# Optimization experiments

Measured on AMD Instinct MI355X. Metric: run time of the kernel, lower is better.

The kernel has to match this reference:

```python
import jax, jax.numpy as jnp
import numpy as np

SIZES = [(64, 32), (32, 16), (16, 8), (8, 16), (16, 32)]
BZ, T, D = 2048, 512, 64


def setup_inputs() -> dict:
    key = jax.random.key(0)
    ks = jax.random.split(key, 32)
    inp = {
        "X": jax.random.normal(ks[0], (BZ, T, D), jnp.float32),
        "missing_mask": (jax.random.uniform(ks[1], (BZ, T, D)) < 0.8).astype(jnp.float32),
        "imputation_latent": jax.random.normal(ks[2], (BZ, T, D), jnp.float32),
    }
    for i, (din, dh) in enumerate(SIZES):
        s = 1.0 / np.sqrt(dh)  # PyTorch RNNCell init range
        k = 3 + 4 * i
        inp[f"wih{i}"] = jax.random.uniform(ks[k], (3 * dh, din), jnp.float32, -s, s)
        inp[f"whh{i}"] = jax.random.uniform(ks[k + 1], (3 * dh, dh), jnp.float32, -s, s)
        inp[f"bih{i}"] = jax.random.uniform(ks[k + 2], (3 * dh,), jnp.float32, -s, s)
        inp[f"bhh{i}"] = jax.random.uniform(ks[k + 3], (3 * dh,), jnp.float32, -s, s)
    so = 1.0 / np.sqrt(32)
    inp["out_w"] = jax.random.uniform(ks[23], (D, 32), jnp.float32, -so, so)
    inp["out_b"] = jax.random.uniform(ks[24], (D,), jnp.float32, -so, so)
    return inp


def _gru_cell(x, h, wih, whh, bih, bhh):
    # PyTorch nn.GRUCell gate order: r, z, n
    gi = x @ wih.T + bih
    gh = h @ whh.T + bhh
    ir, iz, inn = jnp.split(gi, 3, axis=-1)
    hr, hz, hn = jnp.split(gh, 3, axis=-1)
    r = jax.nn.sigmoid(ir + hr)
    z = jax.nn.sigmoid(iz + hz)
    n = jnp.tanh(inn + r * hn)
    return (1.0 - z) * n + z * h


def _forward(X, missing_mask, imputation_latent, params, out_w, out_b):
    imputed = X * missing_mask + imputation_latent * (1.0 - missing_mask)
    xs = jnp.swapaxes(imputed, 0, 1)  # [T, B, D]
    bz = X.shape[0]
    h0 = tuple(jnp.zeros((bz, dh), X.dtype) for _, dh in SIZES)

    def step(hs, x):
        new = []
        inp_x = x
        for i, (wih, whh, bih, bhh) in enumerate(params):
            h = _gru_cell(inp_x, hs[i], wih, whh, bih, bhh)
            new.append(h)
            inp_x = h  # layer i+1 consumes the freshly-updated hidden state
        return tuple(new), new[-1]

    _, hcol = jax.lax.scan(step, h0, xs)  # [T, B, 32]
    hcol = jnp.swapaxes(hcol, 0, 1)  # [B, T, 32]
    return hcol @ out_w.T + out_b


def reference(X, missing_mask, imputation_latent,
              wih0, whh0, bih0, bhh0, wih1, whh1, bih1, bhh1,
              wih2, whh2, bih2, bhh2, wih3, whh3, bih3, bhh3,
              wih4, whh4, bih4, bhh4, out_w, out_b):
    params = [(wih0, whh0, bih0, bhh0), (wih1, whh1, bih1, bhh1),
              (wih2, whh2, bih2, bhh2), (wih3, whh3, bih3, bhh3),
              (wih4, whh4, bih4, bhh4)]
    return _forward(X, missing_mask, imputation_latent, params, out_w, out_b)
```

## Files before the change

kernel.cpp:

```cpp
#include <hip/hip_runtime.h>

typedef short s16x8 __attribute__((ext_vector_type(8)));
typedef short s16x4 __attribute__((ext_vector_type(4)));
typedef float f32x4 __attribute__((ext_vector_type(4)));
typedef unsigned int u32;
typedef unsigned short u16;

#define NT 512
#define DD 64
#define BB 8
#define NTH 512

#define CHUNK 1024

#define P2STRIDE (5*CHUNK)
#define PH0 0
#define PH1 CHUNK
#define PH2 (2*CHUNK)
#define PH3 (3*CHUNK)
#define PH4 (4*CHUNK)
#define FRTOT2 (2*P2STRIDE)
#define NSTEP2 517

#define PSTRIDE (7*CHUNK)
#define XIN0 0
#define H0C (2*CHUNK)
#define H1C (3*CHUNK)
#define H2C (4*CHUNK)
#define H3C (5*CHUNK)
#define H4C (6*CHUNK)
#define FRTOT (2*PSTRIDE)
#define NSTEP_FB 517

#define MFMA16(A,B,C) __builtin_amdgcn_mfma_f32_16x16x32_bf16(A,B,C,0,0,0)

__device__ __forceinline__ float sigf(float x){ return 1.0f/(1.0f+__expf(-x)); }
__device__ __forceinline__ float tanhf2(float x){ return 2.0f/(1.0f+__expf(-2.0f*x)) - 1.0f; }

__device__ __forceinline__ u16 f2bf(float f) {
  u32 u = __builtin_bit_cast(u32, f);
  return (u16)((u + 0x7fffu + ((u >> 16) & 1u)) >> 16);
}
__device__ __forceinline__ float bf2f(u16 h) {
  u32 u = ((u32)h) << 16;
  return __builtin_bit_cast(float, u);
}

__device__ __forceinline__ void soft_barrier() {
  asm volatile("s_waitcnt lgkmcnt(0)" ::: "memory");
  __builtin_amdgcn_s_barrier();
  asm volatile("" ::: "memory");
}

__device__ __forceinline__ u32 cvtpk_bf16(float a, float b) {
  u32 r;
  asm("v_cvt_pk_bf16_f32 %0, %1, %2" : "=v"(r) : "v"(a), "v"(b));
  return r;
}

__device__ __forceinline__ void load_wfrag(const float* __restrict__ W, int row0, int nrow, int din,
                                           int kbase, int lane, s16x8& hi, s16x8& lo)
{
  const int m = lane & 15, kb = lane >> 4;
#pragma unroll
  for (int e = 0; e < 8; ++e) {
    int k = kbase + kb*8 + e;
    float v = (m < nrow && k < din) ? W[(size_t)(row0 + m)*din + k] : 0.0f;
    u16 h = f2bf(v);
    hi[e] = (short)h;
    lo[e] = (short)f2bf(v - bf2f(h));
  }
}

__device__ __forceinline__ void read_b(const u16* base, int lane, s16x8& hi, s16x8& lo)
{
  const int off = ((lane >> 4) << 8) + ((lane & 15) << 3);
  hi = *(const s16x8*)(base + off);
  lo = *(const s16x8*)(base + off + 128);
}

__device__ __forceinline__ void combine_write2(
    f32x4 aR, f32x4 aZ, f32x4 aNi, f32x4 aNh,
    float (&hprev)[4], u16* hdst_base, int jbase, int nrow, int lane)
{
  const int bb = lane & 15, q = lane >> 4;
  float hv[4];
#pragma unroll
  for (int i = 0; i < 4; ++i) {
    float rr = sigf(aR[i]);
    float zz = sigf(aZ[i]);
    float nn = tanhf2(aNi[i] + rr*aNh[i]);
    hv[i] = (1.0f - zz)*nn + zz*hprev[i];
    hprev[i] = hv[i];
  }
  if (bb < 8 && q*4 < nrow) {
    const int j = jbase + q*4;
    u16* dst = hdst_base + ((j >> 3) << 8) + bb*8 + (j & 7);
    u32 p01 = cvtpk_bf16(hv[0], hv[1]);
    u32 p23 = cvtpk_bf16(hv[2], hv[3]);
    float h0 = __builtin_bit_cast(float, p01 << 16);
    float h1 = __builtin_bit_cast(float, p01 & 0xffff0000u);
    float h2 = __builtin_bit_cast(float, p23 << 16);
    float h3 = __builtin_bit_cast(float, p23 & 0xffff0000u);
    u32 q01 = cvtpk_bf16(hv[0]-h0, hv[1]-h1);
    u32 q23 = cvtpk_bf16(hv[2]-h2, hv[3]-h3);
    uint2 hp_; hp_.x = p01; hp_.y = p23;
    uint2 lp_; lp_.x = q01; lp_.y = q23;
    *(uint2*)dst = hp_;
    *(uint2*)(dst + 128) = lp_;
  }
}

__device__ __forceinline__ void combine_write(
    f32x4 aR, f32x4 aZ, f32x4 aNi, f32x4 aNh,
    float (&hprev)[4], u16* hdst_base, int jbase, int nrow, int lane)
{
  const int bb = lane & 15, q = lane >> 4;
  float hv[4];
#pragma unroll
  for (int i = 0; i < 4; ++i) {
    float rr = sigf(aR[i]);
    float zz = sigf(aZ[i]);
    float nn = tanhf2(aNi[i] + rr*aNh[i]);
    hv[i] = (1.0f - zz)*nn + zz*hprev[i];
    hprev[i] = hv[i];
  }
  if (bb < 8 && q*4 < nrow) {
    const int j = jbase + q*4;
    const int kb = j >> 3, e = j & 7;
    s16x4 hh, ll;
#pragma unroll
    for (int i = 0; i < 4; ++i) {
      u16 h = f2bf(hv[i]);
      hh[i] = (short)h;
      ll[i] = (short)f2bf(hv[i] - bf2f(h));
    }
    u16* dst = hdst_base + kb*256 + bb*8 + e;
    *(s16x4*)dst = hh;
    *(s16x4*)(dst + 128) = ll;
  }
}

__global__ __launch_bounds__(256)
void gi0_gemm(const float* __restrict__ X, const float* __restrict__ M, const float* __restrict__ L,
              const float* __restrict__ wih0, const float* __restrict__ bih0,
              const float* __restrict__ bhh0,
              float* __restrict__ gi)
{
  __shared__ u32 xs[128*65];
  const int tid = threadIdx.x;
  const int wv = tid >> 6, lane = tid & 63;
  const int q = lane >> 4;
  const int b = blockIdx.x >> 2;
  const int t0 = (blockIdx.x & 3) * 128;
  const size_t base = ((size_t)b*NT + t0)*DD;

  for (int i = tid; i < 128*64; i += 256) {
    float x = X[base+i], m = M[base+i], l = L[base+i];
    float v = x*m + l*(1.0f - m);
    u16 h = f2bf(v);
    u16 lo2 = f2bf(v - bf2f(h));
    const int t = i >> 6, d = i & 63;
    xs[t*65 + d] = (u32)h | ((u32)lo2 << 16);
  }

  s16x8 Ah[6][2], Al[6][2];
  f32x4 cb[6];
#pragma unroll
  for (int tile = 0; tile < 6; ++tile) {
#pragma unroll
    for (int c = 0; c < 2; ++c)
      load_wfrag(wih0, tile*16, 16, 64, c*32, lane, Ah[tile][c], Al[tile][c]);
#pragma unroll
    for (int i = 0; i < 4; ++i) {
      int row = tile*16 + q*4 + i;
      float bv = bih0[row];
      if (tile < 4) bv += bhh0[row];
      cb[tile][i] = bv;
    }
  }
  __syncthreads();

#pragma unroll
  for (int g2 = 0; g2 < 2; ++g2) {
    const int tloc = g2*64 + wv*16 + (lane & 15);
    s16x8 Bh[2], Bl[2];
#pragma unroll
    for (int c = 0; c < 2; ++c) {
      const u32* p = &xs[tloc*65 + c*32 + q*8];
#pragma unroll
      for (int e = 0; e < 8; ++e) {
        u32 v = p[e];
        Bh[c][e] = (short)(v & 0xffffu);
        Bl[c][e] = (short)(v >> 16);
      }
    }
    float* gp = gi + ((size_t)b*NT + t0 + tloc)*96 + q*4;
#pragma unroll
    for (int tile = 0; tile < 6; ++tile) {
      f32x4 acc = cb[tile];
#pragma unroll
      for (int c = 0; c < 2; ++c) {
        acc = MFMA16(Ah[tile][c], Bh[c], acc);
        acc = MFMA16(Ah[tile][c], Bl[c], acc);
        acc = MFMA16(Al[tile][c], Bh[c], acc);
      }
      *(f32x4*)(gp + tile*16) = acc;
    }
  }
}

__device__ __forceinline__ void wave_l0(
    const float* __restrict__ Whh, const float* __restrict__ bhh,
    const float* __restrict__ gi, int jbase,
    u16* FRu, int b0, int lane)
{
  s16x8 Ahh[3], Ahl[3];
#pragma unroll
  for (int g = 0; g < 3; ++g)
    load_wfrag(Whh, g*32 + jbase, 16, 32, 0, lane, Ahh[g], Ahl[g]);
  const int q = lane >> 4;
  f32x4 cNh;
#pragma unroll
  for (int i = 0; i < 4; ++i) cNh[i] = bhh[64 + jbase + q*4 + i];
  float hprev[4] = {0.f,0.f,0.f,0.f};

  const float* gp = gi + (size_t)(b0 + (lane & 7)) * ((size_t)NT*96) + jbase + q*4;
  f32x4 gR0, gZ0, gN0, gR1, gZ1, gN1;
  gR0 = *(const f32x4*)(gp); gZ0 = *(const f32x4*)(gp+32); gN0 = *(const f32x4*)(gp+64); gp += 96;
  gR1 = *(const f32x4*)(gp); gZ1 = *(const f32x4*)(gp+32); gN1 = *(const f32x4*)(gp+64); gp += 96;

  for (int s = 0; s < NSTEP2; ++s) {
    const int par = s & 1, rp = par ^ 1;
    f32x4 gR2 = {}, gZ2 = {}, gN2 = {};
    if (s + 2 < NT) {
      gR2 = *(const f32x4*)(gp); gZ2 = *(const f32x4*)(gp+32); gN2 = *(const f32x4*)(gp+64); gp += 96;
    }
    if (s < NT) {
      f32x4 aR = gR0, aZ = gZ0, aNi = gN0, aNh = cNh;
      s16x8 bh_, bl_;
      read_b(FRu + rp*P2STRIDE + PH0, lane, bh_, bl_);
      aR  = MFMA16(Ahh[0], bh_, aR);  aR  = MFMA16(Ahh[0], bl_, aR);  aR  = MFMA16(Ahl[0], bh_, aR);
      aZ  = MFMA16(Ahh[1], bh_, aZ);  aZ  = MFMA16(Ahh[1], bl_, aZ);  aZ  = MFMA16(Ahl[1], bh_, aZ);
      aNh = MFMA16(Ahh[2], bh_, aNh); aNh = MFMA16(Ahh[2], bl_, aNh); aNh = MFMA16(Ahl[2], bh_, aNh);
      combine_write2(aR, aZ, aNi, aNh, hprev, FRu + par*P2STRIDE + PH0, jbase, 16, lane);
    }
    gR0 = gR1; gZ0 = gZ1; gN0 = gN1;
    gR1 = gR2; gZ1 = gZ2; gN1 = gN2;
    soft_barrier();
  }
}

template<int DIN, int DH>
__device__ __forceinline__ void wave_mid(
    const float* __restrict__ Wih, const float* __restrict__ Whh,
    const float* __restrict__ bih, const float* __restrict__ bhh,
    int jbase, int xc, int hc, int s0, int s1,
    u16* FRu, int b0, int lane)
{
  const int nrow = (DH - jbase) < 16 ? (DH - jbase) : 16;
  s16x8 Axh[3], Axl[3], Ahh[3], Ahl[3];
#pragma unroll
  for (int g = 0; g < 3; ++g) {
    load_wfrag(Wih, g*DH + jbase, nrow, DIN, 0, lane, Axh[g], Axl[g]);
    load_wfrag(Whh, g*DH + jbase, nrow, DH, 0, lane, Ahh[g], Ahl[g]);
  }
  const int q = lane >> 4;
  f32x4 cR, cZ, cNi, cNh;
#pragma unroll
  for (int i = 0; i < 4; ++i) {
    int lr = q*4 + i;
    int j = jbase + lr;
    bool jr = lr < nrow;
    cR[i]  = jr ? bih[j] + bhh[j] : 0.f;
    cZ[i]  = jr ? bih[DH+j] + bhh[DH+j] : 0.f;
    cNi[i] = jr ? bih[2*DH+j] : 0.f;
    cNh[i] = jr ? bhh[2*DH+j] : 0.f;
  }
  float hprev[4] = {0.f,0.f,0.f,0.f};

  for (int s = 0; s < NSTEP2; ++s) {
    const int par = s & 1, rp = par ^ 1;
    if (s >= s0 && s <= s1) {
      f32x4 aR = cR, aZ = cZ, aNi = cNi, aNh = cNh;
      s16x8 bh_, bl_;
      read_b(FRu + rp*P2STRIDE + xc, lane, bh_, bl_);
      aR  = MFMA16(Axh[0], bh_, aR);  aR  = MFMA16(Axh[0], bl_, aR);  aR  = MFMA16(Axl[0], bh_, aR);
      aZ  = MFMA16(Axh[1], bh_, aZ);  aZ  = MFMA16(Axh[1], bl_, aZ);  aZ  = MFMA16(Axl[1], bh_, aZ);
      aNi = MFMA16(Axh[2], bh_, aNi); aNi = MFMA16(Axh[2], bl_, aNi); aNi = MFMA16(Axl[2], bh_, aNi);
      read_b(FRu + rp*P2STRIDE + hc, lane, bh_, bl_);
      aR  = MFMA16(Ahh[0], bh_, aR);  aR  = MFMA16(Ahh[0], bl_, aR);  aR  = MFMA16(Ahl[0], bh_, aR);
      aZ  = MFMA16(Ahh[1], bh_, aZ);  aZ  = MFMA16(Ahh[1], bl_, aZ);  aZ  = MFMA16(Ahl[1], bh_, aZ);
      aNh = MFMA16(Ahh[2], bh_, aNh); aNh = MFMA16(Ahh[2], bl_, aNh); aNh = MFMA16(Ahl[2], bh_, aNh);
      combine_write2(aR, aZ, aNi, aNh, hprev, FRu + par*P2STRIDE + hc, jbase, nrow, lane);
    }
    soft_barrier();
  }
}

__device__ __forceinline__ void wave_out2(
    const float* __restrict__ OW, const float* __restrict__ OBb,
    u16* FRu, float* __restrict__ out, int b0, int lane)
{
  s16x8 Oh[4], Ol[4];
  f32x4 cO[4];
  const int q = lane >> 4, bb = lane & 15;
#pragma unroll
  for (int t4 = 0; t4 < 4; ++t4) {
    load_wfrag(OW, t4*16, 16, 32, 0, lane, Oh[t4], Ol[t4]);
#pragma unroll
    for (int i = 0; i < 4; ++i) cO[t4][i] = OBb[t4*16 + q*4 + i];
  }
  float* op = out + ((size_t)(b0 + (bb & 7))*NT)*DD + q*4;

  for (int s = 0; s < NSTEP2; ++s) {
    const int rp = (s & 1) ^ 1;
    if (s >= 5) {
      s16x8 bh_, bl_;
      read_b(FRu + rp*P2STRIDE + PH4, lane, bh_, bl_);
#pragma unroll
      for (int t4 = 0; t4 < 4; ++t4) {
        f32x4 a_ = cO[t4];
        a_ = MFMA16(Oh[t4], bh_, a_); a_ = MFMA16(Oh[t4], bl_, a_); a_ = MFMA16(Ol[t4], bh_, a_);
        if (bb < 8) *(f32x4*)(op + t4*16) = a_;
      }
      op += DD;
    }
    soft_barrier();
  }
}

__global__ __launch_bounds__(NTH, 1)
void gru_rec(const float* __restrict__ gi,
             const float* __restrict__ whh0, const float* __restrict__ bhh0,
             const float* __restrict__ wih1, const float* __restrict__ whh1, const float* __restrict__ bih1, const float* __restrict__ bhh1,
             const float* __restrict__ wih2, const float* __restrict__ whh2, const float* __restrict__ bih2, const float* __restrict__ bhh2,
             const float* __restrict__ wih3, const float* __restrict__ whh3, const float* __restrict__ bih3, const float* __restrict__ bhh3,
             const float* __restrict__ wih4, const float* __restrict__ whh4, const float* __restrict__ bih4, const float* __restrict__ bhh4,
             const float* __restrict__ out_w, const float* __restrict__ out_b,
             float* __restrict__ out)
{
  __shared__ __align__(16) u16 FRu[FRTOT2];
  const int tid = threadIdx.x;
  const int w = tid >> 6, lane = tid & 63;
  const int b0 = blockIdx.x * BB;

  for (int i = tid; i < FRTOT2; i += NTH) FRu[i] = 0;
  __syncthreads();

  if (w == 0)
    wave_l0(whh0, bhh0, gi,  0, FRu, b0, lane);
  else if (w == 1)
    wave_l0(whh0, bhh0, gi, 16, FRu, b0, lane);
  else if (w == 2)
    wave_mid<32,16>(wih1,whh1,bih1,bhh1,  0, PH0, PH1, 1, 512, FRu, b0, lane);
  else if (w == 4)
    wave_mid<16, 8>(wih2,whh2,bih2,bhh2,  0, PH1, PH2, 2, 513, FRu, b0, lane);
  else if (w == 5)
    wave_mid< 8,16>(wih3,whh3,bih3,bhh3,  0, PH2, PH3, 3, 514, FRu, b0, lane);
  else if (w == 3)
    wave_mid<16,32>(wih4,whh4,bih4,bhh4,  0, PH3, PH4, 4, 515, FRu, b0, lane);
  else if (w == 6)
    wave_mid<16,32>(wih4,whh4,bih4,bhh4, 16, PH3, PH4, 4, 515, FRu, b0, lane);
  else
    wave_out2(out_w, out_b, FRu, out, b0, lane);
}

__device__ __forceinline__ void write_x(u16* FRu, int par, int w, int lane, float v)
{
  const int d = lane;
  const int chunk = d >> 5, kb = (d >> 3) & 3, e = d & 7;
  u16 h = f2bf(v);
  u16 l2 = f2bf(v - bf2f(h));
  u16* p = FRu + par*PSTRIDE + XIN0 + chunk*CHUNK + kb*256 + w*8 + e;
  p[0] = h; p[128] = l2;
}

template<int DIN, int DH, int NXC>
__device__ __forceinline__ void wave_gru_fb(
    const float* __restrict__ Wih, const float* __restrict__ Whh,
    const float* __restrict__ bih, const float* __restrict__ bhh,
    int jbase, int xc, int hc, int s0, int s1,
    u16* FRu, float* OST,
    const float* __restrict__ X, const float* __restrict__ Mm, const float* __restrict__ Ll,
    float* __restrict__ out, int b0, int w, int lane)
{
  const int nrow = (DH - jbase) < 16 ? (DH - jbase) : 16;
  s16x8 Axh[3][NXC], Axl[3][NXC], Ahh[3], Ahl[3];
#pragma unroll
  for (int g = 0; g < 3; ++g) {
#pragma unroll
    for (int c = 0; c < NXC; ++c)
      load_wfrag(Wih, g*DH + jbase, nrow, DIN, c*32, lane, Axh[g][c], Axl[g][c]);
    load_wfrag(Whh, g*DH + jbase, nrow, DH, 0, lane, Ahh[g], Ahl[g]);
  }
  f32x4 cR, cZ, cNi, cNh;
  {
    const int q = lane >> 4;
#pragma unroll
    for (int i = 0; i < 4; ++i) {
      int lr = q*4 + i;
      int j = jbase + lr;
      bool jr = lr < nrow;
      cR[i]  = jr ? bih[j] + bhh[j] : 0.f;
      cZ[i]  = jr ? bih[DH+j] + bhh[DH+j] : 0.f;
      cNi[i] = jr ? bih[2*DH+j] : 0.f;
      cNh[i] = jr ? bhh[2*DH+j] : 0.f;
    }
  }
  float hprev[4] = {0.f, 0.f, 0.f, 0.f};

  const size_t gbase = ((size_t)(b0 + w))*((size_t)NT*DD) + lane;
  float rx = X[gbase], rm = Mm[gbase], rl = Ll[gbase];
  write_x(FRu, 1, w, lane, rx*rm + rl*(1.0f - rm));
  rx = X[gbase + DD]; rm = Mm[gbase + DD]; rl = Ll[gbase + DD];
  __syncthreads();

  for (int s = 0; s < NSTEP_FB; ++s) {
    const int par = s & 1, rp = par ^ 1;
    float nx = 0.f, nm = 0.f, nl = 0.f;
    if (s <= 509) {
      size_t g = gbase + (size_t)(s+2)*DD;
      nx = X[g]; nm = Mm[g]; nl = Ll[g];
    }
    f32x4 aR = cR, aZ = cZ, aNi = cNi, aNh = cNh;
    const bool run = (s >= s0) && (s <= s1);
    if (run) {
      const u16* RB = FRu + rp*PSTRIDE;
      s16x8 bh_, bl_;
#pragma unroll
      for (int c = 0; c < NXC; ++c) {
        read_b(RB + xc + c*CHUNK, lane, bh_, bl_);
        aR  = MFMA16(Axh[0][c], bh_, aR);  aR  = MFMA16(Axh[0][c], bl_, aR);  aR  = MFMA16(Axl[0][c], bh_, aR);
        aZ  = MFMA16(Axh[1][c], bh_, aZ);  aZ  = MFMA16(Axh[1][c], bl_, aZ);  aZ  = MFMA16(Axl[1][c], bh_, aZ);
        aNi = MFMA16(Axh[2][c], bh_, aNi); aNi = MFMA16(Axh[2][c], bl_, aNi); aNi = MFMA16(Axl[2][c], bh_, aNi);
      }
      read_b(RB + hc, lane, bh_, bl_);
      aR  = MFMA16(Ahh[0], bh_, aR);  aR  = MFMA16(Ahh[0], bl_, aR);  aR  = MFMA16(Ahl[0], bh_, aR);
      aZ  = MFMA16(Ahh[1], bh_, aZ);  aZ  = MFMA16(Ahh[1], bl_, aZ);  aZ  = MFMA16(Ahl[1], bh_, aZ);
      aNh = MFMA16(Ahh[2], bh_, aNh); aNh = MFMA16(Ahh[2], bl_, aNh); aNh = MFMA16(Ahl[2], bh_, aNh);
    }
    __syncthreads();

    if (run)
      combine_write(aR, aZ, aNi, aNh, hprev, FRu + par*PSTRIDE + hc, jbase, nrow, lane);
    if (s >= 5)
      out[((size_t)(b0 + w)*NT + (s-5))*DD + lane] = OST[w*65 + lane];
    if (s <= 510) write_x(FRu, par, w, lane, rx*rm + rl*(1.0f - rm));
    rx = nx; rm = nm; rl = nl;
    __syncthreads();
  }
}

__device__ __forceinline__ void wave_out_fb(
    const float* __restrict__ OW, const float* __restrict__ OBb,
    u16* FRu, float* OST,
    const float* __restrict__ X, const float* __restrict__ Mm, const float* __restrict__ Ll,
    float* __restrict__ out, int b0, int w, int lane)
{
  s16x8 Oh[4], Ol[4];
  f32x4 cO[4];
#pragma unroll
  for (int t4 = 0; t4 < 4; ++t4) {
    load_wfrag(OW, t4*16, 16, 32, 0, lane, Oh[t4], Ol[t4]);
#pragma unroll
    for (int i = 0; i < 4; ++i) cO[t4][i] = OBb[t4*16 + (lane>>4)*4 + i];
  }
  const size_t gbase = ((size_t)(b0 + w))*((size_t)NT*DD) + lane;
  float rx = X[gbase], rm = Mm[gbase], rl = Ll[gbase];
  write_x(FRu, 1, w, lane, rx*rm + rl*(1.0f - rm));
  rx = X[gbase + DD]; rm = Mm[gbase + DD]; rl = Ll[gbase + DD];
  __syncthreads();

  for (int s = 0; s < NSTEP_FB; ++s) {
    const int par = s & 1, rp = par ^ 1;
    float nx = 0.f, nm = 0.f, nl = 0.f;
    if (s <= 509) { size_t g = gbase + (size_t)(s+2)*DD; nx = X[g]; nm = Mm[g]; nl = Ll[g]; }
    if (s >= 5) {
      s16x8 bh_, bl_;
      read_b(FRu + rp*PSTRIDE + H4C, lane, bh_, bl_);
      const int bb = lane & 15, q = lane >> 4;
#pragma unroll
      for (int t4 = 0; t4 < 4; ++t4) {
        f32x4 a_ = cO[t4];
        a_ = MFMA16(Oh[t4], bh_, a_); a_ = MFMA16(Oh[t4], bl_, a_); a_ = MFMA16(Ol[t4], bh_, a_);
        if (bb < 8) {
#pragma unroll
          for (int i = 0; i < 4; ++i) OST[bb*65 + t4*16 + q*4 + i] = a_[i];
        }
      }
    }
    __syncthreads();
    if (s >= 5)
      out[((size_t)(b0 + w)*NT + (s-5))*DD + lane] = OST[w*65 + lane];
    if (s <= 510) write_x(FRu, par, w, lane, rx*rm + rl*(1.0f - rm));
    rx = nx; rm = nm; rl = nl;
    __syncthreads();
  }
}

__global__ __launch_bounds__(NTH, 1)
void gru_mfma(const float* __restrict__ X, const float* __restrict__ M, const float* __restrict__ L,
              const float* __restrict__ wih0, const float* __restrict__ whh0, const float* __restrict__ bih0, const float* __restrict__ bhh0,
              const float* __restrict__ wih1, const float* __restrict__ whh1, const float* __restrict__ bih1, const float* __restrict__ bhh1,
              const float* __restrict__ wih2, const float* __restrict__ whh2, const float* __restrict__ bih2, const float* __restrict__ bhh2,
              const float* __restrict__ wih3, const float* __restrict__ whh3, const float* __restrict__ bih3, const float* __restrict__ bhh3,
              const float* __restrict__ wih4, const float* __restrict__ whh4, const float* __restrict__ bih4, const float* __restrict__ bhh4,
              const float* __restrict__ out_w, const float* __restrict__ out_b,
              float* __restrict__ out)
{
  __shared__ __align__(16) u16 FRu[FRTOT];
  __shared__ float OST[8*65];
  const int tid = threadIdx.x;
  const int w = tid >> 6, lane = tid & 63;
  const int b0 = blockIdx.x * BB;

  for (int i = tid; i < FRTOT; i += NTH) FRu[i] = 0;
  for (int i = tid; i < 8*65; i += NTH) OST[i] = 0.f;
  __syncthreads();

  if (w == 0)
    wave_gru_fb<64,32,2>(wih0,whh0,bih0,bhh0,  0, XIN0, H0C, 0, 511, FRu, OST, X,M,L, out, b0, w, lane);
  else if (w == 1)
    wave_gru_fb<64,32,2>(wih0,whh0,bih0,bhh0, 16, XIN0, H0C, 0, 511, FRu, OST, X,M,L, out, b0, w, lane);
  else if (w == 2)
    wave_gru_fb<32,16,1>(wih1,whh1,bih1,bhh1,  0, H0C,  H1C, 1, 512, FRu, OST, X,M,L, out, b0, w, lane);
  else if (w == 4)
    wave_gru_fb<16, 8,1>(wih2,whh2,bih2,bhh2,  0, H1C,  H2C, 2, 513, FRu, OST, X,M,L, out, b0, w, lane);
  else if (w == 5)
    wave_gru_fb< 8,16,1>(wih3,whh3,bih3,bhh3,  0, H2C,  H3C, 3, 514, FRu, OST, X,M,L, out, b0, w, lane);
  else if (w == 3)
    wave_gru_fb<16,32,1>(wih4,whh4,bih4,bhh4,  0, H3C,  H4C, 4, 515, FRu, OST, X,M,L, out, b0, w, lane);
  else if (w == 6)
    wave_gru_fb<16,32,1>(wih4,whh4,bih4,bhh4, 16, H3C,  H4C, 4, 515, FRu, OST, X,M,L, out, b0, w, lane);
  else
    wave_out_fb(out_w, out_b, FRu, OST, X,M,L, out, b0, w, lane);
}

extern "C" void kernel_launch(void* const* d_in, const int* in_sizes, int n_in,
                              void* d_out, int out_size, void* d_ws, size_t ws_size,
                              hipStream_t stream)
{
  const float* X  = (const float*)d_in[0];
  const float* M  = (const float*)d_in[1];
  const float* L  = (const float*)d_in[2];
  const float* wp[20];
  for (int i = 0; i < 20; ++i) wp[i] = (const float*)d_in[3 + i];
  const float* ow = (const float*)d_in[23];
  const float* ob = (const float*)d_in[24];
  float* out = (float*)d_out;

  const size_t gi_bytes = (size_t)2048 * NT * 96 * sizeof(float);
  if (ws_size >= gi_bytes) {
    float* gi = (float*)d_ws;
    gi0_gemm<<<dim3(2048*4), dim3(256), 0, stream>>>(X, M, L, wp[0], wp[2], wp[3], gi);
    gru_rec<<<dim3(2048 / BB), dim3(NTH), 0, stream>>>(
        gi, wp[1], wp[3],
        wp[4], wp[5], wp[6], wp[7],
        wp[8], wp[9], wp[10], wp[11],
        wp[12], wp[13], wp[14], wp[15],
        wp[16], wp[17], wp[18], wp[19],
        ow, ob, out);
  } else {
    gru_mfma<<<dim3(2048 / BB), dim3(NTH), 0, stream>>>(
        X, M, L,
        wp[0], wp[1], wp[2], wp[3],
        wp[4], wp[5], wp[6], wp[7],
        wp[8], wp[9], wp[10], wp[11],
        wp[12], wp[13], wp[14], wp[15],
        wp[16], wp[17], wp[18], wp[19],
        ow, ob, out);
  }
}
```

Baseline: 840.1 us.

## Pipeline GRU layers across waves in four-timestep super-steps

Replaces the per-timestep wavefront pipeline, where every wave syncs once per timestep, with super-steps of four timesteps per barrier. Each layer wave now computes all 16/32 hidden units and runs the four steps back to back inside one barrier interval. The input projections for four timesteps are batched before the serial hidden recurrence. Layer 4 is split into a wave that computes the input projection into an LDS staging buffer and a wave that runs the recurrence, and the output projection is split across two waves. This cuts barrier count by about four, at the cost of more serial work per wave per interval and larger dynamic LDS use.

```diff
diff --git a/kernel.cpp b/kernel.cpp
--- a/kernel.cpp
+++ b/kernel.cpp
@@ -13,14 +13,12 @@
 
 #define CHUNK 1024
 
-#define P2STRIDE (5*CHUNK)
-#define PH0 0
-#define PH1 CHUNK
-#define PH2 (2*CHUNK)
-#define PH3 (3*CHUNK)
-#define PH4 (4*CHUNK)
-#define FRTOT2 (2*P2STRIDE)
-#define NSTEP2 517
+#define TCH 4096
+#define P3 (5*TCH)
+#define FR3 (2*P3)
+#define XST 6144
+#define LDS3_BYTES (FR3*2 + 2*XST*4)
+#define NSUP 134
 
 #define PSTRIDE (7*CHUNK)
 #define XIN0 0
@@ -77,6 +75,14 @@
   const int off = ((lane >> 4) << 8) + ((lane & 15) << 3);
   hi = *(const s16x8*)(base + off);
   lo = *(const s16x8*)(base + off + 128);
+}
+
+__device__ __forceinline__ void g3(const s16x8& Ah, const s16x8& Al,
+                                   const s16x8& bh, const s16x8& bl, f32x4& acc)
+{
+  acc = MFMA16(Ah, bh, acc);
+  acc = MFMA16(Ah, bl, acc);
+  acc = MFMA16(Al, bh, acc);
 }
 
 __device__ __forceinline__ void combine_write2(
@@ -111,36 +117,6 @@
   }
 }
 
-__device__ __forceinline__ void combine_write(
-    f32x4 aR, f32x4 aZ, f32x4 aNi, f32x4 aNh,
-    float (&hprev)[4], u16* hdst_base, int jbase, int nrow, int lane)
-{
-  const int bb = lane & 15, q = lane >> 4;
-  float hv[4];
-#pragma unroll
-  for (int i = 0; i < 4; ++i) {
-    float rr = sigf(aR[i]);
-    float zz = sigf(aZ[i]);
-    float nn = tanhf2(aNi[i] + rr*aNh[i]);
-    hv[i] = (1.0f - zz)*nn + zz*hprev[i];
-    hprev[i] = hv[i];
-  }
-  if (bb < 8 && q*4 < nrow) {
-    const int j = jbase + q*4;
-    const int kb = j >> 3, e = j & 7;
-    s16x4 hh, ll;
-#pragma unroll
-    for (int i = 0; i < 4; ++i) {
-      u16 h = f2bf(hv[i]);
-      hh[i] = (short)h;
-      ll[i] = (short)f2bf(hv[i] - bf2f(h));
-    }
-    u16* dst = hdst_base + kb*256 + bb*8 + e;
-    *(s16x4*)dst = hh;
-    *(s16x4*)(dst + 128) = ll;
-  }
-}
-
 __global__ __launch_bounds__(256)
 void gi0_gemm(const float* __restrict__ X, const float* __restrict__ M, const float* __restrict__ L,
               const float* __restrict__ wih0, const float* __restrict__ bih0,
@@ -210,160 +186,307 @@
   }
 }
 
-__device__ __forceinline__ void wave_l0(
-    const float* __restrict__ Whh, const float* __restrict__ bhh,
-    const float* __restrict__ gi, int jbase,
-    u16* FRu, int b0, int lane)
-{
-  s16x8 Ahh[3], Ahl[3];
-#pragma unroll
-  for (int g = 0; g < 3; ++g)
-    load_wfrag(Whh, g*32 + jbase, 16, 32, 0, lane, Ahh[g], Ahl[g]);
+__device__ void wv_l0_t4(const float* __restrict__ whh0, const float* __restrict__ bhh0,
+                         const float* __restrict__ gi, u16* FR, int b0, int lane)
+{
+  s16x8 Ahh[2][3], Ahl[2][3];
+#pragma unroll
+  for (int jt = 0; jt < 2; ++jt)
+#pragma unroll
+    for (int g = 0; g < 3; ++g)
+      load_wfrag(whh0, g*32 + jt*16, 16, 32, 0, lane, Ahh[jt][g], Ahl[jt][g]);
   const int q = lane >> 4;
-  f32x4 cNh;
-#pragma unroll
-  for (int i = 0; i < 4; ++i) cNh[i] = bhh[64 + jbase + q*4 + i];
-  float hprev[4] = {0.f,0.f,0.f,0.f};
-
-  const float* gp = gi + (size_t)(b0 + (lane & 7)) * ((size_t)NT*96) + jbase + q*4;
-  f32x4 gR0, gZ0, gN0, gR1, gZ1, gN1;
-  gR0 = *(const f32x4*)(gp); gZ0 = *(const f32x4*)(gp+32); gN0 = *(const f32x4*)(gp+64); gp += 96;
-  gR1 = *(const f32x4*)(gp); gZ1 = *(const f32x4*)(gp+32); gN1 = *(const f32x4*)(gp+64); gp += 96;
-
-  for (int s = 0; s < NSTEP2; ++s) {
-    const int par = s & 1, rp = par ^ 1;
-    f32x4 gR2 = {}, gZ2 = {}, gN2 = {};
-    if (s + 2 < NT) {
-      gR2 = *(const f32x4*)(gp); gZ2 = *(const f32x4*)(gp+32); gN2 = *(const f32x4*)(gp+64); gp += 96;
-    }
-    if (s < NT) {
-      f32x4 aR = gR0, aZ = gZ0, aNi = gN0, aNh = cNh;
-      s16x8 bh_, bl_;
-      read_b(FRu + rp*P2STRIDE + PH0, lane, bh_, bl_);
-      aR  = MFMA16(Ahh[0], bh_, aR);  aR  = MFMA16(Ahh[0], bl_, aR);  aR  = MFMA16(Ahl[0], bh_, aR);
-      aZ  = MFMA16(Ahh[1], bh_, aZ);  aZ  = MFMA16(Ahh[1], bl_, aZ);  aZ  = MFMA16(Ahl[1], bh_, aZ);
-      aNh = MFMA16(Ahh[2], bh_, aNh); aNh = MFMA16(Ahh[2], bl_, aNh); aNh = MFMA16(Ahl[2], bh_, aNh);
-      combine_write2(aR, aZ, aNi, aNh, hprev, FRu + par*P2STRIDE + PH0, jbase, 16, lane);
-    }
-    gR0 = gR1; gZ0 = gZ1; gN0 = gN1;
-    gR1 = gR2; gZ1 = gZ2; gN1 = gN2;
+  f32x4 cNh[2];
+#pragma unroll
+  for (int jt = 0; jt < 2; ++jt)
+#pragma unroll
+    for (int i = 0; i < 4; ++i) cNh[jt][i] = bhh0[64 + jt*16 + q*4 + i];
+  float hp[2][4] = {};
+  const float* gp = gi + (size_t)(b0 + (lane & 7)) * ((size_t)NT*96) + q*4;
+
+  for (int S = 0; S < NSUP; ++S) {
+    const int par = S & 1, rp = par ^ 1;
+    if (S < 128) {
+      const int tb = 4*S;
+      f32x4 g_[4][2][3];
+#pragma unroll
+      for (int t = 0; t < 4; ++t)
+#pragma unroll
+        for (int jt = 0; jt < 2; ++jt) {
+          const float* p = gp + (size_t)(tb + t)*96 + jt*16;
+          g_[t][jt][0] = *(const f32x4*)p;
+          g_[t][jt][1] = *(const f32x4*)(p + 32);
+          g_[t][jt][2] = *(const f32x4*)(p + 64);
+        }
+      const u16* RH = FR + rp*P3 + 0*TCH;
+      u16* WH = FR + par*P3 + 0*TCH;
+      s16x8 hh_, hl_;
+      read_b(RH + 3*1024, lane, hh_, hl_);
+#pragma unroll
+      for (int t = 0; t < 4; ++t) {
+#pragma unroll
+        for (int jt = 0; jt < 2; ++jt) {
+          f32x4 hR = {0.f,0.f,0.f,0.f}, hZ = {0.f,0.f,0.f,0.f}, aNh = cNh[jt];
+          g3(Ahh[jt][0], Ahl[jt][0], hh_, hl_, hR);
+          g3(Ahh[jt][1], Ahl[jt][1], hh_, hl_, hZ);
+          g3(Ahh[jt][2], Ahl[jt][2], hh_, hl_, aNh);
+          f32x4 aR = hR + g_[t][jt][0];
+          f32x4 aZ = hZ + g_[t][jt][1];
+          combine_write2(aR, aZ, g_[t][jt][2], aNh, hp[jt], WH + t*1024, jt*16, 16, lane);
+        }
+        if (t < 3) read_b(WH + t*1024, lane, hh_, hl_);
+      }
+    }
     soft_barrier();
   }
 }
 
 template<int DIN, int DH>
-__device__ __forceinline__ void wave_mid(
-    const float* __restrict__ Wih, const float* __restrict__ Whh,
-    const float* __restrict__ bih, const float* __restrict__ bhh,
-    int jbase, int xc, int hc, int s0, int s1,
-    u16* FRu, int b0, int lane)
-{
-  const int nrow = (DH - jbase) < 16 ? (DH - jbase) : 16;
+__device__ void wv_mid4(const float* __restrict__ Wih, const float* __restrict__ Whh,
+                        const float* __restrict__ bih, const float* __restrict__ bhh,
+                        int cx, int ch, int Sf, u16* FR, int lane)
+{
+  constexpr int nrow = DH < 16 ? DH : 16;
   s16x8 Axh[3], Axl[3], Ahh[3], Ahl[3];
 #pragma unroll
   for (int g = 0; g < 3; ++g) {
-    load_wfrag(Wih, g*DH + jbase, nrow, DIN, 0, lane, Axh[g], Axl[g]);
-    load_wfrag(Whh, g*DH + jbase, nrow, DH, 0, lane, Ahh[g], Ahl[g]);
+    load_wfrag(Wih, g*DH, nrow, DIN, 0, lane, Axh[g], Axl[g]);
+    load_wfrag(Whh, g*DH, nrow, DH, 0, lane, Ahh[g], Ahl[g]);
   }
   const int q = lane >> 4;
   f32x4 cR, cZ, cNi, cNh;
 #pragma unroll
   for (int i = 0; i < 4; ++i) {
-    int lr = q*4 + i;
-    int j = jbase + lr;
-    bool jr = lr < nrow;
+    int j = q*4 + i;
+    bool jr = j < nrow;
     cR[i]  = jr ? bih[j] + bhh[j] : 0.f;
     cZ[i]  = jr ? bih[DH+j] + bhh[DH+j] : 0.f;
     cNi[i] = jr ? bih[2*DH+j] : 0.f;
     cNh[i] = jr ? bhh[2*DH+j] : 0.f;
   }
-  float hprev[4] = {0.f,0.f,0.f,0.f};
-
-  for (int s = 0; s < NSTEP2; ++s) {
-    const int par = s & 1, rp = par ^ 1;
-    if (s >= s0 && s <= s1) {
-      f32x4 aR = cR, aZ = cZ, aNi = cNi, aNh = cNh;
-      s16x8 bh_, bl_;
-      read_b(FRu + rp*P2STRIDE + xc, lane, bh_, bl_);
-      aR  = MFMA16(Axh[0], bh_, aR);  aR  = MFMA16(Axh[0], bl_, aR);  aR  = MFMA16(Axl[0], bh_, aR);
-      aZ  = MFMA16(Axh[1], bh_, aZ);  aZ  = MFMA16(Axh[1], bl_, aZ);  aZ  = MFMA16(Axl[1], bh_, aZ);
-      aNi = MFMA16(Axh[2], bh_, aNi); aNi = MFMA16(Axh[2], bl_, aNi); aNi = MFMA16(Axl[2], bh_, aNi);
-      read_b(FRu + rp*P2STRIDE + hc, lane, bh_, bl_);
-      aR  = MFMA16(Ahh[0], bh_, aR);  aR  = MFMA16(Ahh[0], bl_, aR);  aR  = MFMA16(Ahl[0], bh_, aR);
-      aZ  = MFMA16(Ahh[1], bh_, aZ);  aZ  = MFMA16(Ahh[1], bl_, aZ);  aZ  = MFMA16(Ahl[1], bh_, aZ);
-      aNh = MFMA16(Ahh[2], bh_, aNh); aNh = MFMA16(Ahh[2], bl_, aNh); aNh = MFMA16(Ahl[2], bh_, aNh);
-      combine_write2(aR, aZ, aNi, aNh, hprev, FRu + par*P2STRIDE + hc, jbase, nrow, lane);
+  float hp[4] = {0.f,0.f,0.f,0.f};
+
+  for (int S = 0; S < NSUP; ++S) {
+    const int par = S & 1, rp = par ^ 1;
+    if (S >= Sf && S < Sf + 128) {
+      const u16* RX = FR + rp*P3 + cx*TCH;
+      const u16* RH = FR + rp*P3 + ch*TCH;
+      u16* WH = FR + par*P3 + ch*TCH;
+      s16x8 xh[4], xl[4];
+#pragma unroll
+      for (int t = 0; t < 4; ++t) read_b(RX + t*1024, lane, xh[t], xl[t]);
+      f32x4 aR[4], aZ[4], aNi[4], aNh[4];
+#pragma unroll
+      for (int t = 0; t < 4; ++t) {
+        aR[t] = cR; aZ[t] = cZ; aNi[t] = cNi; aNh[t] = cNh;
+        g3(Axh[0], Axl[0], xh[t], xl[t], aR[t]);
+        g3(Axh[1], Axl[1], xh[t], xl[t], aZ[t]);
+        g3(Axh[2], Axl[2], xh[t], xl[t], aNi[t]);
+      }
+      s16x8 hh_, hl_;
+      read_b(RH + 3*1024, lane, hh_, hl_);
+#pragma unroll
+      for (int t = 0; t < 4; ++t) {
+        g3(Ahh[0], Ahl[0], hh_, hl_, aR[t]);
+        g3(Ahh[1], Ahl[1], hh_, hl_, aZ[t]);
+        g3(Ahh[2], Ahl[2], hh_, hl_, aNh[t]);
+        combine_write2(aR[t], aZ[t], aNi[t], aNh[t], hp, WH + t*1024, 0, nrow, lane);
+        if (t < 3) read_b(WH + t*1024, lane, hh_, hl_);
+      }
     }
     soft_barrier();
   }
 }
 
-__device__ __forceinline__ void wave_out2(
-    const float* __restrict__ OW, const float* __restrict__ OBb,
-    u16* FRu, float* __restrict__ out, int b0, int lane)
-{
-  s16x8 Oh[4], Ol[4];
-  f32x4 cO[4];
+__device__ void wv_l4x(const float* __restrict__ wih4, const float* __restrict__ bih4,
+                       const float* __restrict__ bhh4,
+                       u16* FR, float* XS, int lane)
+{
+  s16x8 Axh[2][3], Axl[2][3];
+#pragma unroll
+  for (int jt = 0; jt < 2; ++jt)
+#pragma unroll
+    for (int g = 0; g < 3; ++g)
+      load_wfrag(wih4, g*32 + jt*16, 16, 16, 0, lane, Axh[jt][g], Axl[jt][g]);
+  const int q = lane >> 4;
+  f32x4 cR[2], cZ[2], cNi[2];
+#pragma unroll
+  for (int jt = 0; jt < 2; ++jt)
+#pragma unroll
+    for (int i = 0; i < 4; ++i) {
+      int j = jt*16 + q*4 + i;
+      cR[jt][i]  = bih4[j] + bhh4[j];
+      cZ[jt][i]  = bih4[32+j] + bhh4[32+j];
+      cNi[jt][i] = bih4[64+j];
+    }
+  for (int S = 0; S < NSUP; ++S) {
+    const int par = S & 1, rp = par ^ 1;
+    if (S >= 4 && S < 4 + 128) {
+      const u16* RX = FR + rp*P3 + 3*TCH;
+      float* XW = XS + par*XST;
+#pragma unroll
+      for (int t = 0; t < 4; ++t) {
+        s16x8 bh_, bl_;
+        read_b(RX + t*1024, lane, bh_, bl_);
+#pragma unroll
+        for (int jt = 0; jt < 2; ++jt) {
+          f32x4 aR = cR[jt], aZ = cZ[jt], aNi = cNi[jt];
+          g3(Axh[jt][0], Axl[jt][0], bh_, bl_, aR);
+          g3(Axh[jt][1], Axl[jt][1], bh_, bl_, aZ);
+          g3(Axh[jt][2], Axl[jt][2], bh_, bl_, aNi);
+          float* w = XW + t*1536 + jt*768 + lane*4;
+          *(f32x4*)(w)       = aR;
+          *(f32x4*)(w + 256) = aZ;
+          *(f32x4*)(w + 512) = aNi;
+        }
+      }
+    }
+    soft_barrier();
+  }
+}
+
+__device__ void wv_l4h(const float* __restrict__ whh4, const float* __restrict__ bhh4,
+                       u16* FR, const float* XS, int lane)
+{
+  s16x8 Ahh[2][3], Ahl[2][3];
+#pragma unroll
+  for (int jt = 0; jt < 2; ++jt)
+#pragma unroll
+    for (int g = 0; g < 3; ++g)
+      load_wfrag(whh4, g*32 + jt*16, 16, 32, 0, lane, Ahh[jt][g], Ahl[jt][g]);
+  const int q = lane >> 4;
+  f32x4 cNh[2];
+#pragma unroll
+  for (int jt = 0; jt < 2; ++jt)
+#pragma unroll
+    for (int i = 0; i < 4; ++i) cNh[jt][i] = bhh4[64 + jt*16 + q*4 + i];
+  float hp[2][4] = {};
+
+  for (int S = 0; S < NSUP; ++S) {
+    const int par = S & 1, rp = par ^ 1;
+    if (S >= 5 && S < 5 + 128) {
+      const float* XR = XS + rp*XST;
+      const u16* RH = FR + rp*P3 + 4*TCH;
+      u16* WH = FR + par*P3 + 4*TCH;
+      s16x8 hh_, hl_;
+      read_b(RH + 3*1024, lane, hh_, hl_);
+#pragma unroll
+      for (int t = 0; t < 4; ++t) {
+#pragma unroll
+        for (int jt = 0; jt < 2; ++jt) {
+          const float* r = XR + t*1536 + jt*768 + lane*4;
+          f32x4 aR  = *(const f32x4*)r;
+          f32x4 aZ  = *(const f32x4*)(r + 256);
+          f32x4 aNi = *(const f32x4*)(r + 512);
+          f32x4 aNh = cNh[jt];
+          g3(Ahh[jt][0], Ahl[jt][0], hh_, hl_, aR);
+          g3(Ahh[jt][1], Ahl[jt][1], hh_, hl_, aZ);
+          g3(Ahh[jt][2], Ahl[jt][2], hh_, hl_, aNh);
+          combine_write2(aR, aZ, aNi, aNh, hp[jt], WH + t*1024, jt*16, 16, lane);
+        }
+        if (t < 3) read_b(WH + t*1024, lane, hh_, hl_);
+      }
+    }
+    soft_barrier();
+  }
+}
+
+__device__ void wv_out4(const float* __restrict__ OW, const float* __restrict__ OBb,
+                        u16* FR, float* __restrict__ out, int b0, int half, int lane)
+{
+  s16x8 Oh[2], Ol[2];
+  f32x4 cO[2];
   const int q = lane >> 4, bb = lane & 15;
 #pragma unroll
-  for (int t4 = 0; t4 < 4; ++t4) {
-    load_wfrag(OW, t4*16, 16, 32, 0, lane, Oh[t4], Ol[t4]);
-#pragma unroll
-    for (int i = 0; i < 4; ++i) cO[t4][i] = OBb[t4*16 + q*4 + i];
-  }
-  float* op = out + ((size_t)(b0 + (bb & 7))*NT)*DD + q*4;
-
-  for (int s = 0; s < NSTEP2; ++s) {
-    const int rp = (s & 1) ^ 1;
-    if (s >= 5) {
-      s16x8 bh_, bl_;
-      read_b(FRu + rp*P2STRIDE + PH4, lane, bh_, bl_);
-#pragma unroll
-      for (int t4 = 0; t4 < 4; ++t4) {
-        f32x4 a_ = cO[t4];
-        a_ = MFMA16(Oh[t4], bh_, a_); a_ = MFMA16(Oh[t4], bl_, a_); a_ = MFMA16(Ol[t4], bh_, a_);
-        if (bb < 8) *(f32x4*)(op + t4*16) = a_;
-      }
-      op += DD;
+  for (int k = 0; k < 2; ++k) {
+    int tile = half*2 + k;
+    load_wfrag(OW, tile*16, 16, 32, 0, lane, Oh[k], Ol[k]);
+#pragma unroll
+    for (int i = 0; i < 4; ++i) cO[k][i] = OBb[tile*16 + q*4 + i];
+  }
+  float* ob = out + ((size_t)(b0 + (bb & 7))*NT)*DD + half*32 + q*4;
+
+  for (int S = 0; S < NSUP; ++S) {
+    const int par = S & 1, rp = par ^ 1;
+    if (S >= 6) {
+      const u16* RH = FR + rp*P3 + 4*TCH;
+      const int tbq = 4*(S - 6);
+#pragma unroll
+      for (int t = 0; t < 4; ++t) {
+        s16x8 bh_, bl_;
+        read_b(RH + t*1024, lane, bh_, bl_);
+        float* op = ob + (size_t)(tbq + t)*DD;
+#pragma unroll
+        for (int k = 0; k < 2; ++k) {
+          f32x4 a_ = cO[k];
+          a_ = MFMA16(Oh[k], bh_, a_); a_ = MFMA16(Oh[k], bl_, a_); a_ = MFMA16(Ol[k], bh_, a_);
+          if (bb < 8) *(f32x4*)(op + k*16) = a_;
+        }
+      }
     }
     soft_barrier();
   }
 }
 
 __global__ __launch_bounds__(NTH, 1)
-void gru_rec(const float* __restrict__ gi,
-             const float* __restrict__ whh0, const float* __restrict__ bhh0,
-             const float* __restrict__ wih1, const float* __restrict__ whh1, const float* __restrict__ bih1, const float* __restrict__ bhh1,
-             const float* __restrict__ wih2, const float* __restrict__ whh2, const float* __restrict__ bih2, const float* __restrict__ bhh2,
-             const float* __restrict__ wih3, const float* __restrict__ whh3, const float* __restrict__ bih3, const float* __restrict__ bhh3,
-             const float* __restrict__ wih4, const float* __restrict__ whh4, const float* __restrict__ bih4, const float* __restrict__ bhh4,
-             const float* __restrict__ out_w, const float* __restrict__ out_b,
-             float* __restrict__ out)
-{
-  __shared__ __align__(16) u16 FRu[FRTOT2];
+void gru_rec_t4(const float* __restrict__ gi,
+                const float* __restrict__ whh0, const float* __restrict__ bhh0,
+                const float* __restrict__ wih1, const float* __restrict__ whh1, const float* __restrict__ bih1, const float* __restrict__ bhh1,
+                const float* __restrict__ wih2, const float* __restrict__ whh2, const float* __restrict__ bih2, const float* __restrict__ bhh2,
+                const float* __restrict__ wih3, const float* __restrict__ whh3, const float* __restrict__ bih3, const float* __restrict__ bhh3,
+                const float* __restrict__ wih4, const float* __restrict__ whh4, const float* __restrict__ bih4, const float* __restrict__ bhh4,
+                const float* __restrict__ out_w, const float* __restrict__ out_b,
+                float* __restrict__ out)
+{
+  extern __shared__ __align__(16) u16 smem_u16[];
+  u16* FR = smem_u16;
+  float* XS = (float*)(smem_u16 + FR3);
   const int tid = threadIdx.x;
   const int w = tid >> 6, lane = tid & 63;
   const int b0 = blockIdx.x * BB;
 
-  for (int i = tid; i < FRTOT2; i += NTH) FRu[i] = 0;
+  for (int i = tid; i < FR3; i += NTH) FR[i] = 0;
+  for (int i = tid; i < 2*XST; i += NTH) XS[i] = 0.f;
   __syncthreads();
 
-  if (w == 0)
-    wave_l0(whh0, bhh0, gi,  0, FRu, b0, lane);
-  else if (w == 1)
-    wave_l0(whh0, bhh0, gi, 16, FRu, b0, lane);
-  else if (w == 2)
-    wave_mid<32,16>(wih1,whh1,bih1,bhh1,  0, PH0, PH1, 1, 512, FRu, b0, lane);
-  else if (w == 4)
-    wave_mid<16, 8>(wih2,whh2,bih2,bhh2,  0, PH1, PH2, 2, 513, FRu, b0, lane);
-  else if (w == 5)
-    wave_mid< 8,16>(wih3,whh3,bih3,bhh3,  0, PH2, PH3, 3, 514, FRu, b0, lane);
-  else if (w == 3)
-    wave_mid<16,32>(wih4,whh4,bih4,bhh4,  0, PH3, PH4, 4, 515, FRu, b0, lane);
-  else if (w == 6)
-    wave_mid<16,32>(wih4,whh4,bih4,bhh4, 16, PH3, PH4, 4, 515, FRu, b0, lane);
-  else
-    wave_out2(out_w, out_b, FRu, out, b0, lane);
+  if (w == 0)      wv_l0_t4(whh0, bhh0, gi, FR, b0, lane);
+  else if (w == 1) wv_mid4<32,16>(wih1, whh1, bih1, bhh1, 0, 1, 1, FR, lane);
+  else if (w == 2) wv_mid4<16, 8>(wih2, whh2, bih2, bhh2, 1, 2, 2, FR, lane);
+  else if (w == 3) wv_mid4< 8,16>(wih3, whh3, bih3, bhh3, 2, 3, 3, FR, lane);
+  else if (w == 4) wv_l4x(wih4, bih4, bhh4, FR, XS, lane);
+  else if (w == 5) wv_l4h(whh4, bhh4, FR, XS, lane);
+  else if (w == 6) wv_out4(out_w, out_b, FR, out, b0, 0, lane);
+  else             wv_out4(out_w, out_b, FR, out, b0, 1, lane);
+}
+
+__device__ __forceinline__ void combine_write(
+    f32x4 aR, f32x4 aZ, f32x4 aNi, f32x4 aNh,
+    float (&hprev)[4], u16* hdst_base, int jbase, int nrow, int lane)
+{
+  const int bb = lane & 15, q = lane >> 4;
+  float hv[4];
+#pragma unroll
+  for (int i = 0; i < 4; ++i) {
+    float rr = sigf(aR[i]);
+    float zz = sigf(aZ[i]);
+    float nn = tanhf2(aNi[i] + rr*aNh[i]);
+    hv[i] = (1.0f - zz)*nn + zz*hprev[i];
+    hprev[i] = hv[i];
+  }
+  if (bb < 8 && q*4 < nrow) {
+    const int j = jbase + q*4;
+    const int kb = j >> 3, e = j & 7;
+    s16x4 hh, ll;
+#pragma unroll
+    for (int i = 0; i < 4; ++i) {
+      u16 h = f2bf(hv[i]);
+      hh[i] = (short)h;
+      ll[i] = (short)f2bf(hv[i] - bf2f(h));
+    }
+    u16* dst = hdst_base + kb*256 + bb*8 + e;
+    *(s16x4*)dst = hh;
+    *(s16x4*)(dst + 128) = ll;
+  }
 }
 
 __device__ __forceinline__ void write_x(u16* FRu, int par, int w, int lane, float v)
@@ -513,7 +636,7 @@
   __shared__ float OST[8*65];
   const int tid = threadIdx.x;
   const int w = tid >> 6, lane = tid & 63;
-  const int b0 = blockIdx.x * BB;
+  const int b0 = blockIdx.x * 8;
 
   for (int i = tid; i < FRTOT; i += NTH) FRu[i] = 0;
   for (int i = tid; i < 8*65; i += NTH) OST[i] = 0.f;
@@ -554,7 +677,8 @@
   if (ws_size >= gi_bytes) {
     float* gi = (float*)d_ws;
     gi0_gemm<<<dim3(2048*4), dim3(256), 0, stream>>>(X, M, L, wp[0], wp[2], wp[3], gi);
-    gru_rec<<<dim3(2048 / BB), dim3(NTH), 0, stream>>>(
+    hipFuncSetAttribute((const void*)gru_rec_t4, hipFuncAttributeMaxDynamicSharedMemorySize, LDS3_BYTES);
+    gru_rec_t4<<<dim3(2048 / BB), dim3(NTH), LDS3_BYTES, stream>>>(
         gi, wp[1], wp[3],
         wp[4], wp[5], wp[6], wp[7],
         wp[8], wp[9], wp[10], wp[11],
```

Result: slower. 1.043 ms (+24.1%).
